# Kernel optimization log

Hardware: AMD Instinct MI355X
Metric: run time of the kernel (lower is better)

## Reference

```python
import math
import jax, jax.numpy as jnp
import numpy as np

B, S, E = 4, 2048, 768
H, D = 12, 64
LOCAL_H, GLOBAL_H = 8, 4
WINDOW_BASE, MIN_W, MAX_W = 128, 32, 512
GLOBAL_RATIO = 0.1
MASK_VALUE = -1e9


def setup_inputs() -> dict:
    key = jax.random.key(0)
    k1, k2, k3 = jax.random.split(key, 3)
    return {
        "x": jax.random.normal(k1, (B, S, E), dtype=jnp.float32),
        "w_attn": jax.random.normal(k2, (E, 3 * E), dtype=jnp.float32) * 0.02,
        "b_attn": jnp.zeros((3 * E,), dtype=jnp.float32),
        "w_proj": jax.random.normal(k3, (E, E), dtype=jnp.float32) * 0.02,
        "b_proj": jnp.zeros((E,), dtype=jnp.float32),
    }


def _masks(seq_len: int):
    # dynamic window (adaptive): base * sqrt(S/base), clamped
    w = int(WINDOW_BASE * math.sqrt(seq_len / WINDOW_BASE))
    w = max(MIN_W, min(w, MAX_W))
    half = w // 2
    i = jnp.arange(seq_len)[:, None]
    j = jnp.arange(seq_len)[None, :]
    # local: window band then causal override -> allowed iff i-half <= j <= i
    local_allowed = (j >= i - half) & (j <= i)
    local_mask = jnp.where(local_allowed, 0.0, MASK_VALUE).astype(jnp.float32)
    # global: columns at linspace positions allowed for all rows, plus full causal
    n_glob = max(1, int(seq_len * GLOBAL_RATIO))
    gpos = jnp.linspace(0.0, seq_len - 1, n_glob).astype(jnp.int32)
    is_gcol = jnp.zeros((seq_len,), dtype=bool).at[gpos].set(True)
    global_allowed = (j <= i) | is_gcol[None, :]
    global_mask = jnp.where(global_allowed, 0.0, MASK_VALUE).astype(jnp.float32)
    return local_mask, global_mask


def _attend(q, k, v, mask):
    # q,k,v: [B,h,S,D]; mask: [S,S]
    scale = 1.0 / math.sqrt(q.shape[-1])
    scores = jnp.einsum("bhqd,bhkd->bhqk", q, k) * scale + mask[None, None]
    w = jax.nn.softmax(scores, axis=-1)
    return jnp.einsum("bhqk,bhkd->bhqd", w, v)


def reference(x, w_attn, b_attn, w_proj, b_proj):
    b, s, _ = x.shape
    qkv = x @ w_attn + b_attn                       # [B,S,3E]
    q, k, v = jnp.split(qkv, 3, axis=-1)
    def heads(t):
        return t.reshape(b, s, H, D).transpose(0, 2, 1, 3)  # [B,H,S,D]
    q, k, v = heads(q), heads(k), heads(v)
    local_mask, global_mask = _masks(s)
    local_out = _attend(q[:, :LOCAL_H], k[:, :LOCAL_H], v[:, :LOCAL_H], local_mask)
    global_out = _attend(q[:, LOCAL_H:], k[:, LOCAL_H:], v[:, LOCAL_H:], global_mask)
    attn = jnp.concatenate([local_out, global_out], axis=1)  # heads 0..7 local, 8..11 global
    attn = attn.transpose(0, 2, 1, 3).reshape(b, s, E)
    return attn @ w_proj + b_proj
```

## Files before the change

kernel.cpp:

```cpp
#include <hip/hip_runtime.h>
#include <stdint.h>


#define NH 12
#define SQ 2048

typedef __bf16 bf16x8 __attribute__((ext_vector_type(8)));
typedef float f32x4 __attribute__((ext_vector_type(4)));

#define GLOAD_LDS16(g, l)                                                      \
  __builtin_amdgcn_global_load_lds(                                            \
      (__attribute__((address_space(1))) void*)(g),                            \
      (__attribute__((address_space(3))) void*)(l), 16, 0, 0)

__device__ __forceinline__ unsigned short bfbits(float f) {
  __bf16 h = (__bf16)f;
  return *(unsigned short*)&h;
}

__global__ __launch_bounds__(256) void prep(
    const float* __restrict__ x, unsigned short* __restrict__ xb,
    const float* __restrict__ w_attn, unsigned short* __restrict__ wattnT,
    const float* __restrict__ w_proj, unsigned short* __restrict__ wprojT) {
  const int bid = blockIdx.x, t = threadIdx.x;
  if (bid < 512) {
    const int n4 = 8192 * 768 / 4;
    for (int i = bid * 256 + t; i < n4; i += 512 * 256) {
      float4 v = ((const float4*)x)[i];
      ((ushort4*)xb)[i] = make_ushort4(bfbits(v.x), bfbits(v.y), bfbits(v.z), bfbits(v.w));
    }
    return;
  }
  __shared__ float tile[32][33];
  const float* in; unsigned short* out; int K, N, tl;
  if (bid < 512 + 72 * 24) { in = w_attn; out = wattnT; K = 768; N = 2304; tl = bid - 512; }
  else                     { in = w_proj; out = wprojT; K = 768; N = 768;  tl = bid - 512 - 72 * 24; }
  const int tpr = N / 32;
  const int n0 = (tl % tpr) * 32, k0 = (tl / tpr) * 32;
  const int tx = t & 31, ty = t >> 5;
  for (int r = ty; r < 32; r += 8) tile[r][tx] = in[(size_t)(k0 + r) * N + n0 + tx];
  __syncthreads();
  for (int r = ty; r < 32; r += 8) out[(size_t)(n0 + r) * K + k0 + tx] = bfbits(tile[tx][r]);
}

__global__ __launch_bounds__(256) void vprep(const unsigned short* __restrict__ QKV,
                                             unsigned short* __restrict__ Vtb,
                                             unsigned short* __restrict__ Kg,
                                             unsigned short* __restrict__ VgT,
                                             int* __restrict__ gidx) {
  const int id = blockIdx.x, t = threadIdx.x;
  if (id < 1536) {
    const int bh = id >> 5, b = bh / NH, h = bh % NH;
    const int s0 = (id & 31) * 64;
    __shared__ unsigned short T[64][72];
    const int r = t >> 2, c0 = (t & 3) * 16;
    const size_t src = (size_t)(b * SQ + s0 + r) * 2304 + 1536 + h * 64 + c0;
    *(uint4*)&T[r][c0]     = *(const uint4*)&QKV[src];
    *(uint4*)&T[r][c0 + 8] = *(const uint4*)&QKV[src + 8];
    __syncthreads();
    unsigned short pk[16];
#pragma unroll
    for (int z = 0; z < 16; ++z) pk[z] = T[c0 + z][r];
    size_t dst = (size_t)bh * 131072 + (size_t)r * 2048 + s0 + c0;
    *(uint4*)&Vtb[dst]     = *(uint4*)&pk[0];
    *(uint4*)&Vtb[dst + 8] = *(uint4*)&pk[8];
    return;
  }
  const int g = id - 1536;
  const int bh = g >> 3, y = g & 7;
  const int b = bh >> 2, h = 8 + (bh & 3);
  if (g == 0) {
    int c = t;
    gidx[c] = (c < 203) ? (int)((double)c * (2047.0 / 203.0)) : ((c == 203) ? 2047 : -1);
  }
  {
    int c = t, ch = y;
    int col = (c < 203) ? (int)((double)c * (2047.0 / 203.0)) : ((c == 203) ? 2047 : -1);
    uint4 v = {0u, 0u, 0u, 0u};
    if (col >= 0) v = *(const uint4*)&QKV[(size_t)(b * SQ + col) * 2304 + 768 + h * 64 + ch * 8];
    *(uint4*)&Kg[((size_t)bh * 256 + c) * 64 + ch * 8] = v;
  }
  {
    int d = t >> 2;
    int cb = (t & 3) * 64 + y * 8;
    for (int cc = 0; cc < 8; ++cc) {
      int c = cb + cc;
      int col = (c < 203) ? (int)((double)c * (2047.0 / 203.0)) : ((c == 203) ? 2047 : -1);
      unsigned short v = 0;
      if (col >= 0) v = QKV[(size_t)(b * SQ + col) * 2304 + 1536 + h * 64 + d];
      VgT[((size_t)bh * 64 + d) * 256 + c] = v;
    }
  }
}

__device__ __forceinline__ void gemm_mainloop(
    const unsigned short* __restrict__ A, const unsigned short* __restrict__ BT,
    int m0, int n0, int tid,
    unsigned short* As, unsigned short* Bs,
    f32x4 acc[4][4]) {
  const int lane = tid & 63, wave = tid >> 6;
  const int wm = wave >> 1, wn = wave & 1;
  const int ln = lane & 15, quad = lane >> 4, ln7 = lane & 7;
  const int srow = tid >> 3;
  const int scol = ((tid & 7) ^ (srow & 7)) * 8;
  const int sbase = wave * 512;

#pragma unroll
  for (int mi = 0; mi < 4; ++mi)
#pragma unroll
    for (int ni = 0; ni < 4; ++ni) acc[mi][ni] = (f32x4){0.f, 0.f, 0.f, 0.f};

  auto stage = [&](int kt, int buf) {
    const int k0 = kt * 64;
    const int bo = buf * 8192;
#pragma unroll
    for (int rr = 0; rr < 4; ++rr) {
      GLOAD_LDS16(A  + (size_t)(m0 + rr * 32 + srow) * 768 + k0 + scol,
                  &As[bo + rr * 2048 + sbase]);
      GLOAD_LDS16(BT + (size_t)(n0 + rr * 32 + srow) * 768 + k0 + scol,
                  &Bs[bo + rr * 2048 + sbase]);
    }
  };

  stage(0, 0);
  int buf = 0;
  for (int kt = 0; kt < 12; ++kt) {
    stage(kt < 11 ? kt + 1 : 11, buf ^ 1);
    asm volatile("s_waitcnt vmcnt(8)" ::: "memory");
    __builtin_amdgcn_sched_barrier(0);
    __builtin_amdgcn_s_barrier();
    __builtin_amdgcn_s_setprio(1);
    const int bo = buf * 8192;
#pragma unroll
    for (int kh = 0; kh < 2; ++kh) {
      const int sk = ((kh * 4 + quad) ^ ln7) * 8;
      bf16x8 aF[4], bF[4];
#pragma unroll
      for (int mi = 0; mi < 4; ++mi)
        aF[mi] = *(const bf16x8*)&As[bo + (wm * 64 + mi * 16 + ln) * 64 + sk];
#pragma unroll
      for (int ni = 0; ni < 4; ++ni)
        bF[ni] = *(const bf16x8*)&Bs[bo + (wn * 64 + ni * 16 + ln) * 64 + sk];
#pragma unroll
      for (int mi = 0; mi < 4; ++mi)
#pragma unroll
        for (int ni = 0; ni < 4; ++ni)
          acc[mi][ni] = __builtin_amdgcn_mfma_f32_16x16x32_bf16(aF[mi], bF[ni], acc[mi][ni], 0, 0, 0);
    }
    __builtin_amdgcn_s_setprio(0);
    asm volatile("s_waitcnt lgkmcnt(0)" ::: "memory");
    __builtin_amdgcn_sched_barrier(0);
    __builtin_amdgcn_s_barrier();
    buf ^= 1;
  }
}

__global__ __launch_bounds__(256, 2) void qkv_gemm(
    const unsigned short* __restrict__ Xb, const unsigned short* __restrict__ WT,
    const float* __restrict__ bias, unsigned short* __restrict__ Out) {
  __shared__ __attribute__((aligned(16))) unsigned short As[2 * 128 * 64];
  __shared__ __attribute__((aligned(16))) unsigned short Bs[2 * 128 * 64];
  f32x4 acc[4][4];
  const int wg = (blockIdx.x & 7) * 144 + (blockIdx.x >> 3);
  const int m0 = (wg / 18) * 128, n0 = (wg % 18) * 128;
  const int tid = threadIdx.x;
  gemm_mainloop(Xb, WT, m0, n0, tid, As, Bs, acc);
  const int lane = tid & 63, wave = tid >> 6;
  const int wm = wave >> 1, wn = wave & 1, ln = lane & 15, quad = lane >> 4;
#pragma unroll
  for (int mi = 0; mi < 4; ++mi)
#pragma unroll
    for (int ni = 0; ni < 4; ++ni) {
      int n = n0 + wn * 64 + ni * 16 + ln;
      float bs = bias[n];
#pragma unroll
      for (int rg = 0; rg < 4; ++rg) {
        int m = m0 + wm * 64 + mi * 16 + quad * 4 + rg;
        Out[(size_t)m * 2304 + n] = bfbits(acc[mi][ni][rg] + bs);
      }
    }
}

__global__ __launch_bounds__(256, 2) void proj_gemm(
    const unsigned short* __restrict__ Ab, const unsigned short* __restrict__ WT,
    const float* __restrict__ bias, float* __restrict__ Out) {
  __shared__ __attribute__((aligned(16))) unsigned short As[2 * 128 * 64];
  __shared__ __attribute__((aligned(16))) unsigned short Bs[2 * 128 * 64];
  f32x4 acc[4][4];
  const int wg = (blockIdx.x & 7) * 48 + (blockIdx.x >> 3);
  const int m0 = (wg / 6) * 128, n0 = (wg % 6) * 128;
  const int tid = threadIdx.x;
  gemm_mainloop(Ab, WT, m0, n0, tid, As, Bs, acc);
  const int lane = tid & 63, wave = tid >> 6;
  const int wm = wave >> 1, wn = wave & 1, ln = lane & 15, quad = lane >> 4;
#pragma unroll
  for (int mi = 0; mi < 4; ++mi)
#pragma unroll
    for (int ni = 0; ni < 4; ++ni)
#pragma unroll
      for (int rg = 0; rg < 4; ++rg) {
        int m = m0 + wm * 64 + mi * 16 + quad * 4 + rg;
        int n = n0 + wn * 64 + ni * 16 + ln;
        Out[(size_t)m * 768 + n] = acc[mi][ni][rg] + bias[n];
      }
}

__global__ __launch_bounds__(256, 4) void attn_kernel(
    const unsigned short* __restrict__ QKV,
    const unsigned short* __restrict__ Vtb,
    const unsigned short* __restrict__ Kg, const unsigned short* __restrict__ VgT,
    const int* __restrict__ gidx,
    unsigned short* __restrict__ AOut,
    unsigned short* __restrict__ Opart,
    float* __restrict__ Lpart) {
  __shared__ __attribute__((aligned(16))) unsigned short Ks[64 * 64];
  __shared__ __attribute__((aligned(16))) unsigned short Vs[64 * 64];
  __shared__ __attribute__((aligned(16))) unsigned short Ps[64 * 64];

  const int gid = blockIdx.x;
  int b, h, qb, vt0, vt1;
  bool multi = false;
  if (gid < 1536) {
    int bh = gid / 96, rem = gid % 96;
    b = bh >> 2; h = 8 + (bh & 3);
    int part;
    if (rem < 4)       { qb = rem;                               part = 0; }
    else if (rem < 20) { int z = rem - 4;  qb = 4 + (z >> 1);    part = z & 1; }
    else if (rem < 44) { int z = rem - 20; int q = z / 3; qb = 12 + q; part = z - 3 * q; }
    else if (rem < 76) { int z = rem - 44; qb = 20 + (z >> 2);   part = z & 3; }
    else               { int z = rem - 76; int q = z / 5; qb = 28 + q; part = z - 5 * q; }
    vt0 = part * 8;
    vt1 = min(vt0 + 8, qb + 5);
    multi = (qb >= 4);
  } else {
    int lid = gid - 1536;
    int bh = lid >> 5; b = bh >> 3; h = bh & 7; qb = lid & 31;
    vt0 = ((qb > 4) ? qb - 4 : 0) + 4;
    vt1 = qb + 5;
  }
  const int qb0 = qb * 64;
  const bool is_local = (h < 8);
  const int tid = threadIdx.x, lane = tid & 63, wave = tid >> 6;
  const int ln = lane & 15, quad = lane >> 4;
  const int bh48 = b * NH + h;
  const int bhg = (b << 2) | (h & 3);

  const size_t qoff = (size_t)(b * SQ + qb0 + wave * 16 + ln) * 2304 + h * 64;
  bf16x8 qA0 = *(const bf16x8*)&QKV[qoff + quad * 8];
  bf16x8 qA1 = *(const bf16x8*)&QKV[qoff + 32 + quad * 8];

  bf16x8 onesF;
#pragma unroll
  for (int z = 0; z < 8; ++z) onesF[z] = (__bf16)1.0f;

  f32x4 o[4];
  f32x4 ls = (f32x4){0.f, 0.f, 0.f, 0.f};
#pragma unroll
  for (int dt = 0; dt < 4; ++dt) o[dt] = (f32x4){0.f, 0.f, 0.f, 0.f};

  const int irow = qb0 + wave * 16 + quad * 4;
  const int iw = qb0 + wave * 16;
  const int sr = tid >> 3, sch = tid & 7;
  const int ssw = (sch ^ (sr & 7)) * 8;
  const int s0k = (quad ^ (ln & 7)) * 8;
  const int s1k = ((quad + 4) ^ (ln & 7)) * 8;
  const int lnh = ln >> 3, ln7 = ln & 7;

  const float S2 = 0.125f * 1.44269504f, B2 = 8.0f * 1.44269504f;

  uint4 pk0, pk1, pv0, pv1;
  auto issue_load = [&](int vt) {
    if (vt >= 4) {
      const int kstart = (vt - 4) * 64;
      const size_t ko = (size_t)(b * SQ + kstart + sr) * 2304 + 768 + h * 64 + sch * 8;
      pk0 = *(const uint4*)&QKV[ko];
      pk1 = *(const uint4*)&QKV[ko + (size_t)32 * 2304];
      const size_t vo = (size_t)bh48 * 131072 + (size_t)sr * 2048 + kstart + sch * 8;
      pv0 = *(const uint4*)&Vtb[vo];
      pv1 = *(const uint4*)&Vtb[vo + 32 * 2048];
    } else {
      const int kg0 = vt * 64;
      pk0 = *(const uint4*)&Kg[((size_t)bhg * 256 + kg0 + sr) * 64 + sch * 8];
      pk1 = *(const uint4*)&Kg[((size_t)bhg * 256 + kg0 + 32 + sr) * 64 + sch * 8];
      pv0 = *(const uint4*)&VgT[((size_t)bhg * 64 + sr) * 256 + kg0 + sch * 8];
      pv1 = *(const uint4*)&VgT[((size_t)bhg * 64 + 32 + sr) * 256 + kg0 + sch * 8];
    }
  };
  issue_load(vt0);

  for (int vt = vt0; vt < vt1; ++vt) {
    const bool gph = (vt < 4);
    __syncthreads();
    *(uint4*)&Ks[sr * 64 + ssw]        = pk0;
    *(uint4*)&Ks[(32 + sr) * 64 + ssw] = pk1;
    *(uint4*)&Vs[sr * 64 + ssw]        = pv0;
    *(uint4*)&Vs[(32 + sr) * 64 + ssw] = pv1;
    __syncthreads();
    if (vt + 1 < vt1) issue_load(vt + 1);

    const int kstart = (vt - 4) * 64;
    const int kg0 = vt * 64;
    float sc[4][4];
    const bool full = !gph && (kstart + 63 <= iw) && (!is_local || kstart >= iw - 241);
#pragma unroll
    for (int nt = 0; nt < 4; ++nt) {
      bf16x8 kF0 = *(const bf16x8*)&Ks[(nt * 16 + ln) * 64 + s0k];
      bf16x8 kF1 = *(const bf16x8*)&Ks[(nt * 16 + ln) * 64 + s1k];
      f32x4 c = (f32x4){0.f, 0.f, 0.f, 0.f};
      c = __builtin_amdgcn_mfma_f32_16x16x32_bf16(qA0, kF0, c, 0, 0, 0);
      c = __builtin_amdgcn_mfma_f32_16x16x32_bf16(qA1, kF1, c, 0, 0, 0);
      if (full) {
#pragma unroll
        for (int rg = 0; rg < 4; ++rg) sc[nt][rg] = c[rg] * S2 - B2;
      } else if (!gph) {
        int j = kstart + nt * 16 + ln;
#pragma unroll
        for (int rg = 0; rg < 4; ++rg) {
          int i = irow + rg;
          bool ok = is_local ? (j >= i - 256 && j <= i) : (j <= i);
          sc[nt][rg] = ok ? (c[rg] * S2 - B2) : -1e9f;
        }
      } else {
        int jg = gidx[kg0 + nt * 16 + ln];
#pragma unroll
        for (int rg = 0; rg < 4; ++rg) {
          bool ok = jg > (irow + rg);
          sc[nt][rg] = ok ? (c[rg] * S2 - B2) : -1e9f;
        }
      }
    }

    __bf16* P = (__bf16*)Ps;
#pragma unroll
    for (int rg = 0; rg < 4; ++rg) {
      int prow = wave * 16 + quad * 4 + rg;
      int pbase = prow * 64 + ln7;
      int pr7 = prow & 7;
#pragma unroll
      for (int nt = 0; nt < 4; ++nt)
        P[pbase + (((nt * 2 + lnh) ^ pr7) << 3)] = (__bf16)exp2f(sc[nt][rg]);
    }
    bf16x8 pF0 = *(const bf16x8*)&Ps[(wave * 16 + ln) * 64 + s0k];
    bf16x8 pF1 = *(const bf16x8*)&Ps[(wave * 16 + ln) * 64 + s1k];
    ls = __builtin_amdgcn_mfma_f32_16x16x32_bf16(pF0, onesF, ls, 0, 0, 0);
    ls = __builtin_amdgcn_mfma_f32_16x16x32_bf16(pF1, onesF, ls, 0, 0, 0);
#pragma unroll
    for (int dt = 0; dt < 4; ++dt) {
      bf16x8 vF0 = *(const bf16x8*)&Vs[(dt * 16 + ln) * 64 + s0k];
      bf16x8 vF1 = *(const bf16x8*)&Vs[(dt * 16 + ln) * 64 + s1k];
      o[dt] = __builtin_amdgcn_mfma_f32_16x16x32_bf16(pF0, vF0, o[dt], 0, 0, 0);
      o[dt] = __builtin_amdgcn_mfma_f32_16x16x32_bf16(pF1, vF1, o[dt], 0, 0, 0);
    }
  }

  if (gid >= 1536 || !multi) {
#pragma unroll
    for (int dt = 0; dt < 4; ++dt)
#pragma unroll
      for (int rg = 0; rg < 4; ++rg) {
        int row = b * SQ + qb0 + wave * 16 + quad * 4 + rg;
        int e = h * 64 + dt * 16 + ln;
        AOut[(size_t)row * 768 + e] = bfbits(o[dt][rg] / ls[rg]);
      }
  } else {
#pragma unroll
    for (int dt = 0; dt < 4; ++dt)
#pragma unroll
      for (int rg = 0; rg < 4; ++rg) {
        int row = wave * 16 + quad * 4 + rg;
        Opart[(size_t)gid * 4096 + row * 64 + dt * 16 + ln] = bfbits(o[dt][rg]);
      }
    if (ln == 0) {
#pragma unroll
      for (int rg = 0; rg < 4; ++rg)
        Lpart[(size_t)gid * 64 + wave * 16 + quad * 4 + rg] = ls[rg];
    }
  }
}

__global__ __launch_bounds__(256) void combine_parts(
    const unsigned short* __restrict__ Opart, const float* __restrict__ Lpart,
    unsigned short* __restrict__ AOut) {
  const int bid = blockIdx.x;
  const int bh = bid / 28, qb = bid % 28 + 4;
  const int b = bh >> 2, h = 8 + (bh & 3);
  int C, np;
  if (qb < 12)      { C = 2 * qb - 4;  np = 2; }
  else if (qb < 20) { C = 3 * qb - 16; np = 3; }
  else if (qb < 28) { C = 4 * qb - 36; np = 4; }
  else              { C = 5 * qb - 64; np = 5; }
  const int slot0 = bh * 96 + C;
  const int t = threadIdx.x, r = t >> 2, c0 = (t & 3) * 16;
  float acc[16];
#pragma unroll
  for (int z = 0; z < 16; ++z) acc[z] = 0.f;
  float l = 0.f;
  for (int p = 0; p < np; ++p) {
    const unsigned short* src = &Opart[(size_t)(slot0 + p) * 4096 + r * 64 + c0];
    bf16x8 v0 = *(const bf16x8*)&src[0];
    bf16x8 v1 = *(const bf16x8*)&src[8];
#pragma unroll
    for (int z = 0; z < 8; ++z) { acc[z] += (float)v0[z]; acc[8 + z] += (float)v1[z]; }
    l += Lpart[(size_t)(slot0 + p) * 64 + r];
  }
  float inv = 1.f / l;
  unsigned short pk[16];
#pragma unroll
  for (int z = 0; z < 16; ++z) pk[z] = bfbits(acc[z] * inv);
  size_t dst = (size_t)(b * SQ + qb * 64 + r) * 768 + h * 64 + c0;
  *(uint4*)&AOut[dst]     = *(uint4*)&pk[0];
  *(uint4*)&AOut[dst + 8] = *(uint4*)&pk[8];
}

extern "C" void kernel_launch(void* const* d_in, const int* in_sizes, int n_in,
                              void* d_out, int out_size, void* d_ws, size_t ws_size,
                              hipStream_t stream) {
  const float* x      = (const float*)d_in[0];
  const float* w_attn = (const float*)d_in[1];
  const float* b_attn = (const float*)d_in[2];
  const float* w_proj = (const float*)d_in[3];
  const float* b_proj = (const float*)d_in[4];
  float* out = (float*)d_out;

  char* ws = (char*)d_ws;
  size_t off = 0;
  auto alloc = [&](size_t bytes) {
    void* p = ws + off;
    off += (bytes + 255) & ~(size_t)255;
    return p;
  };
  unsigned short* xb     = (unsigned short*)alloc((size_t)8192 * 768 * 2);
  unsigned short* wattnT = (unsigned short*)alloc((size_t)2304 * 768 * 2);
  unsigned short* wprojT = (unsigned short*)alloc((size_t)768 * 768 * 2);
  unsigned short* qkvb   = (unsigned short*)alloc((size_t)8192 * 2304 * 2);
  unsigned short* Vtb    = (unsigned short*)alloc((size_t)48 * 64 * 2048 * 2);
  unsigned short* Kgb    = (unsigned short*)alloc((size_t)16 * 256 * 64 * 2);
  unsigned short* VgTb   = (unsigned short*)alloc((size_t)16 * 64 * 256 * 2);
  int* gidxb             = (int*)alloc((size_t)256 * 4);
  unsigned short* Opartb = (unsigned short*)alloc((size_t)1536 * 4096 * 2);
  float* Lpartb          = (float*)alloc((size_t)1536 * 64 * 4);
  unsigned short* attnb  = xb;

  prep<<<dim3(512 + 72 * 24 + 24 * 24), dim3(256), 0, stream>>>(
      x, xb, w_attn, wattnT, w_proj, wprojT);
  qkv_gemm<<<dim3(1152), dim3(256), 0, stream>>>(xb, wattnT, b_attn, qkvb);
  vprep<<<dim3(1536 + 128), dim3(256), 0, stream>>>(qkvb, Vtb, Kgb, VgTb, gidxb);
  attn_kernel<<<dim3(2560), dim3(256), 0, stream>>>(qkvb, Vtb, Kgb, VgTb, gidxb,
                                                    attnb, Opartb, Lpartb);
  combine_parts<<<dim3(448), dim3(256), 0, stream>>>(Opartb, Lpartb, attnb);
  proj_gemm<<<dim3(384), dim3(256), 0, stream>>>(attnb, wprojT, b_proj, out);
}
```

Before: 209.0 us.

## Fuse V transpose into QKV GEMM epilogue, trim pipeline tail and setprio

The QKV GEMM epilogue now writes V columns straight into the transposed per-head layout (Vtb) instead of storing them to the QKV buffer, so vprep no longer runs its 1536 transpose blocks and only builds the global K/V gather. The gathered V for the global heads is now read from Vtb. The GEMM main loop also drops the redundant last-iteration stage reload and the s_setprio calls. The transposed stores are strided 4-byte writes along key rows, which may coalesce less well than the original row-major stores.

```diff
diff --git a/kernel.cpp b/kernel.cpp
--- a/kernel.cpp
+++ b/kernel.cpp
@@ -44,31 +44,14 @@
 }
 
 __global__ __launch_bounds__(256) void vprep(const unsigned short* __restrict__ QKV,
-                                             unsigned short* __restrict__ Vtb,
+                                             const unsigned short* __restrict__ Vtb,
                                              unsigned short* __restrict__ Kg,
                                              unsigned short* __restrict__ VgT,
                                              int* __restrict__ gidx) {
-  const int id = blockIdx.x, t = threadIdx.x;
-  if (id < 1536) {
-    const int bh = id >> 5, b = bh / NH, h = bh % NH;
-    const int s0 = (id & 31) * 64;
-    __shared__ unsigned short T[64][72];
-    const int r = t >> 2, c0 = (t & 3) * 16;
-    const size_t src = (size_t)(b * SQ + s0 + r) * 2304 + 1536 + h * 64 + c0;
-    *(uint4*)&T[r][c0]     = *(const uint4*)&QKV[src];
-    *(uint4*)&T[r][c0 + 8] = *(const uint4*)&QKV[src + 8];
-    __syncthreads();
-    unsigned short pk[16];
-#pragma unroll
-    for (int z = 0; z < 16; ++z) pk[z] = T[c0 + z][r];
-    size_t dst = (size_t)bh * 131072 + (size_t)r * 2048 + s0 + c0;
-    *(uint4*)&Vtb[dst]     = *(uint4*)&pk[0];
-    *(uint4*)&Vtb[dst + 8] = *(uint4*)&pk[8];
-    return;
-  }
-  const int g = id - 1536;
+  const int g = blockIdx.x, t = threadIdx.x;
   const int bh = g >> 3, y = g & 7;
   const int b = bh >> 2, h = 8 + (bh & 3);
+  const int bh48 = b * NH + h;
   if (g == 0) {
     int c = t;
     gidx[c] = (c < 203) ? (int)((double)c * (2047.0 / 203.0)) : ((c == 203) ? 2047 : -1);
@@ -87,7 +70,7 @@
       int c = cb + cc;
       int col = (c < 203) ? (int)((double)c * (2047.0 / 203.0)) : ((c == 203) ? 2047 : -1);
       unsigned short v = 0;
-      if (col >= 0) v = QKV[(size_t)(b * SQ + col) * 2304 + 1536 + h * 64 + d];
+      if (col >= 0) v = Vtb[(size_t)bh48 * 131072 + (size_t)d * 2048 + col];
       VgT[((size_t)bh * 64 + d) * 256 + c] = v;
     }
   }
@@ -125,11 +108,14 @@
   stage(0, 0);
   int buf = 0;
   for (int kt = 0; kt < 12; ++kt) {
-    stage(kt < 11 ? kt + 1 : 11, buf ^ 1);
-    asm volatile("s_waitcnt vmcnt(8)" ::: "memory");
+    if (kt < 11) {
+      stage(kt + 1, buf ^ 1);
+      asm volatile("s_waitcnt vmcnt(8)" ::: "memory");
+    } else {
+      asm volatile("s_waitcnt vmcnt(0)" ::: "memory");
+    }
     __builtin_amdgcn_sched_barrier(0);
     __builtin_amdgcn_s_barrier();
-    __builtin_amdgcn_s_setprio(1);
     const int bo = buf * 8192;
 #pragma unroll
     for (int kh = 0; kh < 2; ++kh) {
@@ -147,7 +133,6 @@
         for (int ni = 0; ni < 4; ++ni)
           acc[mi][ni] = __builtin_amdgcn_mfma_f32_16x16x32_bf16(aF[mi], bF[ni], acc[mi][ni], 0, 0, 0);
     }
-    __builtin_amdgcn_s_setprio(0);
     asm volatile("s_waitcnt lgkmcnt(0)" ::: "memory");
     __builtin_amdgcn_sched_barrier(0);
     __builtin_amdgcn_s_barrier();
@@ -157,7 +142,8 @@
 
 __global__ __launch_bounds__(256, 2) void qkv_gemm(
     const unsigned short* __restrict__ Xb, const unsigned short* __restrict__ WT,
-    const float* __restrict__ bias, unsigned short* __restrict__ Out) {
+    const float* __restrict__ bias, unsigned short* __restrict__ Out,
+    unsigned short* __restrict__ Vtb) {
   __shared__ __attribute__((aligned(16))) unsigned short As[2 * 128 * 64];
   __shared__ __attribute__((aligned(16))) unsigned short Bs[2 * 128 * 64];
   f32x4 acc[4][4];
@@ -167,18 +153,40 @@
   gemm_mainloop(Xb, WT, m0, n0, tid, As, Bs, acc);
   const int lane = tid & 63, wave = tid >> 6;
   const int wm = wave >> 1, wn = wave & 1, ln = lane & 15, quad = lane >> 4;
-#pragma unroll
-  for (int mi = 0; mi < 4; ++mi)
+  if (n0 < 1536) {
+#pragma unroll
+    for (int mi = 0; mi < 4; ++mi)
+#pragma unroll
+      for (int ni = 0; ni < 4; ++ni) {
+        int n = n0 + wn * 64 + ni * 16 + ln;
+        float bs = bias[n];
+#pragma unroll
+        for (int rg = 0; rg < 4; ++rg) {
+          int m = m0 + wm * 64 + mi * 16 + quad * 4 + rg;
+          Out[(size_t)m * 2304 + n] = bfbits(acc[mi][ni][rg] + bs);
+        }
+      }
+  } else {
+    const int bb = m0 >> 11;
+    const int key0 = (m0 & 2047) + wm * 64;
 #pragma unroll
     for (int ni = 0; ni < 4; ++ni) {
-      int n = n0 + wn * 64 + ni * 16 + ln;
-      float bs = bias[n];
-#pragma unroll
-      for (int rg = 0; rg < 4; ++rg) {
-        int m = m0 + wm * 64 + mi * 16 + quad * 4 + rg;
-        Out[(size_t)m * 2304 + n] = bfbits(acc[mi][ni][rg] + bs);
-      }
-    }
+      int e = (n0 - 1536) + wn * 64 + ni * 16 + ln;
+      int h = e >> 6, d = e & 63;
+      float bs = bias[1536 + e];
+      size_t rowb = (size_t)(bb * NH + h) * 131072 + (size_t)d * 2048;
+#pragma unroll
+      for (int mi = 0; mi < 4; ++mi) {
+        int key = key0 + mi * 16 + quad * 4;
+        unsigned int w0 = (unsigned int)bfbits(acc[mi][ni][0] + bs) |
+                          ((unsigned int)bfbits(acc[mi][ni][1] + bs) << 16);
+        unsigned int w1 = (unsigned int)bfbits(acc[mi][ni][2] + bs) |
+                          ((unsigned int)bfbits(acc[mi][ni][3] + bs) << 16);
+        *(unsigned int*)&Vtb[rowb + key]     = w0;
+        *(unsigned int*)&Vtb[rowb + key + 2] = w1;
+      }
+    }
+  }
 }
 
 __global__ __launch_bounds__(256, 2) void proj_gemm(
@@ -443,8 +451,8 @@
 
   prep<<<dim3(512 + 72 * 24 + 24 * 24), dim3(256), 0, stream>>>(
       x, xb, w_attn, wattnT, w_proj, wprojT);
-  qkv_gemm<<<dim3(1152), dim3(256), 0, stream>>>(xb, wattnT, b_attn, qkvb);
-  vprep<<<dim3(1536 + 128), dim3(256), 0, stream>>>(qkvb, Vtb, Kgb, VgTb, gidxb);
+  qkv_gemm<<<dim3(1152), dim3(256), 0, stream>>>(xb, wattnT, b_attn, qkvb, Vtb);
+  vprep<<<dim3(128), dim3(256), 0, stream>>>(qkvb, Vtb, Kgb, VgTb, gidxb);
   attn_kernel<<<dim3(2560), dim3(256), 0, stream>>>(qkvb, Vtb, Kgb, VgTb, gidxb,
                                                     attnb, Opartb, Lpartb);
   combine_parts<<<dim3(448), dim3(256), 0, stream>>>(Opartb, Lpartb, attnb);
```

After: 205.3 us. No clear change (-1.8%).
